# Optimization experiments

Hardware: AMD Instinct MI355X
Metric: run time of the kernel (lower is better)

The kernel has to match this reference:

```python
import jax, jax.numpy as jnp
import numpy as np

B, T, S = 2, 1024, 1024
D_Q, D_KV, D_OUT = 2048, 2048, 2048
N_Q, N_KV, H = 16, 4, 128
G = N_Q // N_KV  # GQA groups
MIN_TS, MAX_TS = 1.0, 10000.0
SDPA_SCALE = 1.0  # dia uses scale=1.0 in F.scaled_dot_product_attention


def setup_inputs() -> dict:
    key = jax.random.key(0)
    ks = jax.random.split(key, 6)
    Xq = jax.random.normal(ks[0], (B, T, D_Q), jnp.float32)
    Xkv = jax.random.normal(ks[1], (B, S, D_KV), jnp.float32)
    q_positions = jnp.broadcast_to(jnp.arange(T, dtype=jnp.int32), (B, T))
    kv_positions = jnp.broadcast_to(jnp.arange(S, dtype=jnp.int32), (B, S))
    Wq = jax.random.normal(ks[2], (D_Q, N_Q, H), jnp.float32) * (D_Q ** -0.5)
    Wk = jax.random.normal(ks[3], (D_KV, N_KV, H), jnp.float32) * (D_KV ** -0.5)
    Wv = jax.random.normal(ks[4], (D_KV, N_KV, H), jnp.float32) * (D_KV ** -0.5)
    Wo = jax.random.normal(ks[5], (N_Q, H, D_OUT), jnp.float32) * ((N_Q * H) ** -0.5)
    return {"Xq": Xq, "Xkv": Xkv, "q_positions": q_positions,
            "kv_positions": kv_positions, "Wq": Wq, "Wk": Wk, "Wv": Wv, "Wo": Wo}


def _apply_rope(x, positions):
    # x: (B, L, N, H); positions: (B, L) int
    half = H // 2
    fraction = 2.0 * jnp.arange(half, dtype=jnp.float32) / H
    timescale = MIN_TS * (MAX_TS / MIN_TS) ** fraction  # (half,)
    sinusoid = positions.astype(jnp.float32)[:, :, None, None] / timescale  # (B,L,1,half)
    sin, cos = jnp.sin(sinusoid), jnp.cos(sinusoid)
    x = x.astype(jnp.float32)
    x1, x2 = jnp.split(x, 2, axis=-1)
    return jnp.concatenate([x1 * cos - x2 * sin, x2 * cos + x1 * sin], axis=-1)


def reference(Xq, Xkv, q_positions, kv_positions, Wq, Wk, Wv, Wo):
    # QKV projections (DenseGeneral): (B,L,D) x (D,N,H) -> (B,L,N,H)
    q = jnp.einsum('btd,dnh->btnh', Xq, Wq)
    k = jnp.einsum('bsd,dnh->bsnh', Xkv, Wk)
    v = jnp.einsum('bsd,dnh->bsnh', Xkv, Wv)
    # RoPE on q and k
    q = _apply_rope(q, q_positions)
    k = _apply_rope(k, kv_positions)
    # GQA attention, scale = 1.0 (as in dia), no mask, non-causal
    q = q.transpose(0, 2, 1, 3).reshape(B, N_KV, G, T, H)  # (B,K,G,T,H)
    k = k.transpose(0, 2, 1, 3)                             # (B,K,S,H)
    v = v.transpose(0, 2, 1, 3)                             # (B,K,S,H)
    scores = jnp.einsum('bkgth,bksh->bkgts', q, k) * SDPA_SCALE
    probs = jax.nn.softmax(scores, axis=-1)
    attn = jnp.einsum('bkgts,bksh->bkgth', probs, v)        # (B,K,G,T,H)
    attn = attn.reshape(B, N_Q, T, H).transpose(0, 2, 1, 3)  # (B,T,N,H)
    # Output projection (DenseGeneral contracting (N,H))
    out = jnp.einsum('btnh,nho->bto', attn, Wo)
    return out
```

## Files before the change

kernel.cpp:

```cpp
#include <hip/hip_runtime.h>
#include <hip/hip_bf16.h>
#include <math.h>
#include <stdint.h>

#define B_SZ 2
#define T_SZ 1024
#define S_SZ 1024
#define NQ 16
#define NKV 4
#define HD 128
#define DQ 2048
#define DKV 2048
#define DOUT 2048

typedef _Float16 half8 __attribute__((ext_vector_type(8)));
typedef _Float16 half4 __attribute__((ext_vector_type(4)));
typedef float f32x4 __attribute__((ext_vector_type(4)));

__device__ __forceinline__ half8 load8_f16(const _Float16* p) {
    return *reinterpret_cast<const half8*>(p);
}

__device__ __forceinline__ void stage16(const _Float16* g, _Float16* l, int lane) {
#if __has_builtin(__builtin_amdgcn_global_load_lds)
    __builtin_amdgcn_global_load_lds(
        (const __attribute__((address_space(1))) uint32_t*)g,
        (__attribute__((address_space(3))) uint32_t*)l, 16, 0, 0);
#else
    *reinterpret_cast<half8*>(l + lane * 8) = *reinterpret_cast<const half8*>(g);
#endif
}

__device__ __forceinline__ void conv_blk(const float* __restrict__ in,
                                         _Float16* __restrict__ out, int vb) {
    size_t i = ((size_t)vb * 256 + threadIdx.x) * 8;
    float4 a = *reinterpret_cast<const float4*>(in + i);
    float4 b = *reinterpret_cast<const float4*>(in + i + 4);
    half8 r;
    r[0] = (_Float16)a.x; r[1] = (_Float16)a.y; r[2] = (_Float16)a.z; r[3] = (_Float16)a.w;
    r[4] = (_Float16)b.x; r[5] = (_Float16)b.y; r[6] = (_Float16)b.z; r[7] = (_Float16)b.w;
    *reinterpret_cast<half8*>(out + i) = r;
}

__device__ __forceinline__ void tr_blk(const float* __restrict__ in,
                                       _Float16* __restrict__ out,
                                       int R, int C, int bx, int by,
                                       _Float16 (*tile)[72]) {
    const int tx = threadIdx.x & 15, ty = threadIdx.x >> 4;
    const int r0 = by * 64, c0 = bx * 64;
    #pragma unroll
    for (int i = 0; i < 4; ++i) {
        int r = ty + i * 16;
        float4 v = *reinterpret_cast<const float4*>(&in[(size_t)(r0 + r) * C + c0 + tx * 4]);
        tile[r][tx * 4 + 0] = (_Float16)v.x;
        tile[r][tx * 4 + 1] = (_Float16)v.y;
        tile[r][tx * 4 + 2] = (_Float16)v.z;
        tile[r][tx * 4 + 3] = (_Float16)v.w;
    }
    __syncthreads();
    #pragma unroll
    for (int i = 0; i < 4; ++i) {
        int oc = ty + i * 16;
        half4 v;
        v[0] = tile[tx * 4 + 0][oc];
        v[1] = tile[tx * 4 + 1][oc];
        v[2] = tile[tx * 4 + 2][oc];
        v[3] = tile[tx * 4 + 3][oc];
        *reinterpret_cast<half4*>(&out[(size_t)(c0 + oc) * R + r0 + tx * 4]) = v;
    }
}

__device__ __forceinline__ void tr16_blk(const _Float16* __restrict__ in,
                                         _Float16* __restrict__ out,
                                         int Cin, int Cout, int r0, int c0,
                                         _Float16 (*tile)[72]) {
    const int tx = threadIdx.x & 15, ty = threadIdx.x >> 4;
    #pragma unroll
    for (int i = 0; i < 4; ++i) {
        int r = ty + i * 16;
        half4 v = *reinterpret_cast<const half4*>(&in[(size_t)(r0 + r) * Cin + c0 + tx * 4]);
        tile[r][tx * 4 + 0] = v[0];
        tile[r][tx * 4 + 1] = v[1];
        tile[r][tx * 4 + 2] = v[2];
        tile[r][tx * 4 + 3] = v[3];
    }
    __syncthreads();
    #pragma unroll
    for (int i = 0; i < 4; ++i) {
        int oc = ty + i * 16;
        half4 v;
        v[0] = tile[tx * 4 + 0][oc];
        v[1] = tile[tx * 4 + 1][oc];
        v[2] = tile[tx * 4 + 2][oc];
        v[3] = tile[tx * 4 + 3][oc];
        *reinterpret_cast<half4*>(&out[(size_t)(c0 + oc) * Cout + r0 + tx * 4]) = v;
    }
}

__device__ __forceinline__ void rope_blk(_Float16* __restrict__ x,
                                         const int* __restrict__ pos,
                                         int N, int rowStride, int vb) {
    size_t idx = (size_t)vb * 256 + threadIdx.x;
    int h = (int)(idx & 63);
    size_t g = idx >> 6;
    int n = (int)(g % (size_t)N);
    size_t bl = g / (size_t)N;
    float p = (float)pos[bl];
    float ts = powf(10000.f, (float)h * (1.f / 64.f));
    float ang = p / ts;
    float s = sinf(ang), c = cosf(ang);
    size_t base = bl * (size_t)rowStride + (size_t)n * HD;
    float x1 = (float)x[base + h];
    float x2 = (float)x[base + h + 64];
    x[base + h]      = (_Float16)(x1 * c - x2 * s);
    x[base + h + 64] = (_Float16)(x2 * c + x1 * s);
}

__global__ __launch_bounds__(256) void prep1(const float* __restrict__ Xq, _Float16* __restrict__ Xq16,
                                             const float* __restrict__ Xkv, _Float16* __restrict__ Xkv16,
                                             const float* __restrict__ Wq, _Float16* __restrict__ WqT,
                                             const float* __restrict__ Wk, const float* __restrict__ Wv,
                                             _Float16* __restrict__ WkvT) {
    __shared__ _Float16 tile[64][72];
    int bx = blockIdx.x;
    if (bx < 2048) { conv_blk(Xq, Xq16, bx); return; }
    bx -= 2048;
    if (bx < 2048) { conv_blk(Xkv, Xkv16, bx); return; }
    bx -= 2048;
    if (bx < 1024) { tr_blk(Wq, WqT, 2048, 2048, bx & 31, bx >> 5, tile); return; }
    bx -= 1024;
    if (bx < 256) { tr_blk(Wk, WkvT, 2048, 512, bx & 7, bx >> 3, tile); return; }
    bx -= 256;
    tr_blk(Wv, WkvT + (size_t)512 * 2048, 2048, 512, bx & 7, bx >> 3, tile);
}

__global__ __launch_bounds__(256) void prep2(const float* __restrict__ Wo, _Float16* __restrict__ WoT,
                                             _Float16* __restrict__ Qh, const int* __restrict__ qpos,
                                             _Float16* __restrict__ KVh, const int* __restrict__ kpos,
                                             _Float16* __restrict__ VTh) {
    __shared__ _Float16 tile[64][72];
    int bx = blockIdx.x;
    if (bx < 1024) { tr_blk(Wo, WoT, 2048, 2048, bx & 31, bx >> 5, tile); return; }
    bx -= 1024;
    if (bx < 8192) { rope_blk(Qh, qpos, NQ, NQ * HD, bx); return; }
    bx -= 8192;
    if (bx < 2048) { rope_blk(KVh, kpos, NKV, 1024, bx); return; }
    bx -= 2048;
    {
        const int head = bx >> 5;
        const int t = bx & 31;
        const int sx = t & 15, hx = t >> 4;
        const int b = head >> 2, kn = head & 3;
        const _Float16* in = KVh + (size_t)(b * S_SZ) * 1024 + 512 + kn * HD;
        _Float16* out = VTh + (size_t)head * HD * S_SZ;
        tr16_blk(in, out, 1024, 1024, sx * 64, hx * 64, tile);
    }
}

template <int BM, int BN, typename TC>
__device__ __forceinline__ void gemm_tile(const _Float16* __restrict__ A,
                                          const _Float16* __restrict__ Bt,
                                          TC* __restrict__ C,
                                          int N, int K, int kbeg, int kend,
                                          int bm, int bn, _Float16* lds) {
    constexpr int ASEG = BM / 8, BSEG = BN / 8, TSEG = ASEG + BSEG, PSEG = TSEG / 4;
    constexpr int BUFSZ = TSEG * 512;
    const int tid = threadIdx.x, lane = tid & 63, w = tid >> 6;
    const int quad = lane >> 4, l16 = lane & 15;
    constexpr int WM = BM / 2, WN = BN / 2, MI = WM / 16, NI = WN / 16;
    const int wm = (w >> 1) * WM, wn = (w & 1) * WN;

    const int srl = lane >> 3;
    const int skb = (lane & 7) ^ srl;

    const _Float16* gp[PSEG];
    _Float16* lp[PSEG];
    #pragma unroll
    for (int p = 0; p < PSEG; ++p) {
        int s = w + p * 4;
        if (s < ASEG) {
            gp[p] = A + (size_t)(bm + s * 8 + srl) * K + kbeg + skb * 8;
        } else {
            gp[p] = Bt + (size_t)(bn + (s - ASEG) * 8 + srl) * K + kbeg + skb * 8;
        }
        lp[p] = lds + s * 512;
    }

    f32x4 acc[MI][NI];
    #pragma unroll
    for (int i = 0; i < MI; ++i)
        #pragma unroll
        for (int j = 0; j < NI; ++j)
            acc[i][j] = (f32x4){0.f, 0.f, 0.f, 0.f};

    const int nsteps = (kend - kbeg) >> 6;

    #pragma unroll
    for (int p = 0; p < PSEG; ++p)
        stage16(gp[p], lp[p], lane);
    __syncthreads();

    const int rxa = l16 & 7;
    int cur = 0;
    for (int it = 0; it < nsteps; ++it) {
        if (it + 1 < nsteps) {
            const int ko = (it + 1) * 64;
            const int nb = (cur ^ 1) * BUFSZ;
            #pragma unroll
            for (int p = 0; p < PSEG; ++p)
                stage16(gp[p] + ko, lp[p] + nb, lane);
        }
        const _Float16* lb = lds + cur * BUFSZ;
        #pragma unroll
        for (int h = 0; h < 2; ++h) {
            const int kb0 = h * 4 + quad;
            const int kswz = (kb0 ^ rxa) * 8;
            half8 af[MI], bf[NI];
            #pragma unroll
            for (int i = 0; i < MI; ++i) {
                const int r = wm + 16 * i + l16;
                af[i] = *reinterpret_cast<const half8*>(&lb[r * 64 + kswz]);
            }
            #pragma unroll
            for (int j = 0; j < NI; ++j) {
                const int r = wn + 16 * j + l16;
                bf[j] = *reinterpret_cast<const half8*>(&lb[BM * 64 + r * 64 + kswz]);
            }
            #pragma unroll
            for (int i = 0; i < MI; ++i)
                #pragma unroll
                for (int j = 0; j < NI; ++j)
                    acc[i][j] = __builtin_amdgcn_mfma_f32_16x16x32_f16(af[i], bf[j], acc[i][j], 0, 0, 0);
        }
        __syncthreads();
        cur ^= 1;
    }

    #pragma unroll
    for (int i = 0; i < MI; ++i)
        #pragma unroll
        for (int j = 0; j < NI; ++j)
            #pragma unroll
            for (int r = 0; r < 4; ++r) {
                size_t idx = (size_t)(bm + wm + 16 * i + quad * 4 + r) * N + bn + wn + 16 * j + l16;
                C[idx] = (TC)acc[i][j][r];
            }
}

__global__ __launch_bounds__(256) void proj_fused(const _Float16* __restrict__ Xq,
                                                  const _Float16* __restrict__ WqT,
                                                  _Float16* __restrict__ Qh,
                                                  const _Float16* __restrict__ Xkv,
                                                  const _Float16* __restrict__ WkvT,
                                                  _Float16* __restrict__ KVh) {
    __shared__ __align__(16) _Float16 lds[2 * (128 + 64) * 64];
    int bx = blockIdx.x;
    if (bx < 512) {
        gemm_tile<128, 64, _Float16>(Xq, WqT, Qh, 2048, 2048, 0, 2048,
                                     (bx & 15) * 128, (bx >> 4) * 64, lds);
    } else {
        bx -= 512;
        gemm_tile<128, 64, _Float16>(Xkv, WkvT, KVh, 1024, 2048, 0, 2048,
                                     (bx & 15) * 128, (bx >> 4) * 64, lds);
    }
}

__global__ __launch_bounds__(256) void gemm_out(const _Float16* __restrict__ A,
                                                const _Float16* __restrict__ Bt,
                                                float* __restrict__ C) {
    __shared__ __align__(16) _Float16 lds[2 * (128 + 64) * 64];
    const int bx = blockIdx.x;
    gemm_tile<128, 64, float>(A, Bt, C, 2048, 2048, 0, 2048,
                              (bx & 15) * 128, (bx >> 4) * 64, lds);
}

__global__ __launch_bounds__(256) void attn_kernel(const _Float16* __restrict__ Q,
                                                   const _Float16* __restrict__ KV,
                                                   const _Float16* __restrict__ VT,
                                                   _Float16* __restrict__ O) {
    constexpr int KBUF = 64 * 128;
    constexpr int VBUF = 128 * 64;
    constexpr int BUFSZ = KBUF + VBUF;
    __shared__ __align__(16) _Float16 lds[2 * BUFSZ];
    __shared__ __align__(16) _Float16 Ps[4][16][72];
    const int tid = threadIdx.x, lane = tid & 63, w = tid >> 6;
    const int quad = lane >> 4, l16 = lane & 15;
    const int blk = blockIdx.x;
    const int t0 = (blk & 15) * 64;
    const int n  = (blk >> 4) & 15;
    const int b  = blk >> 8;
    const int kn = n >> 2;
    const _Float16* KVb  = KV + (size_t)b * S_SZ * 1024 + kn * HD;
    const _Float16* Vhead = VT + (size_t)(b * NKV + kn) * HD * S_SZ;

    const int krow_i = lane >> 4;
    const int kcp    = lane & 15;
    const int vrow_i = lane >> 3;
    const int vcp    = lane & 7;

    half8 qf[4];
    #pragma unroll
    for (int kh = 0; kh < 4; ++kh)
        qf[kh] = load8_f16(&Q[(((size_t)b * T_SZ + t0 + w * 16 + l16) * NQ + n) * HD + kh * 32 + quad * 8]);

    f32x4 o_acc[8];
    #pragma unroll
    for (int i = 0; i < 8; ++i) o_acc[i] = (f32x4){0.f, 0.f, 0.f, 0.f};
    float m_row[4] = {-1e30f, -1e30f, -1e30f, -1e30f};
    float l_part[4] = {0.f, 0.f, 0.f, 0.f};

    auto stage_tile = [&](int s0, int buf) {
        _Float16* kb = lds + buf * BUFSZ;
        _Float16* vb = kb + KBUF;
        #pragma unroll
        for (int j = 0; j < 4; ++j) {
            const int s = w + j * 4;
            const int row = 4 * s + krow_i;
            const int kc = kcp ^ (row & 7);
            stage16(KVb + (size_t)(s0 + row) * 1024 + kc * 8, kb + s * 512, lane);
        }
        #pragma unroll
        for (int j = 0; j < 4; ++j) {
            const int s = w + j * 4;
            const int row = 8 * s + vrow_i;
            const int vc = vcp ^ (row & 7);
            stage16(Vhead + (size_t)row * S_SZ + s0 + vc * 8, vb + s * 512, lane);
        }
    };

    stage_tile(0, 0);
    __syncthreads();

    const int rx = l16 & 7;
    int cur = 0;
    for (int t = 0; t < S_SZ / 64; ++t) {
        if (t + 1 < S_SZ / 64)
            stage_tile((t + 1) * 64, cur ^ 1);
        const _Float16* Kb = lds + cur * BUFSZ;
        const _Float16* Vb = Kb + KBUF;

        f32x4 sf[4];
        __builtin_amdgcn_s_setprio(1);
        #pragma unroll
        for (int i4 = 0; i4 < 4; ++i4) {
            const int srow = i4 * 16 + l16;
            f32x4 sa = (f32x4){0.f, 0.f, 0.f, 0.f};
            #pragma unroll
            for (int kh = 0; kh < 4; ++kh) {
                const int c = kh * 4 + quad;
                half8 bk = *reinterpret_cast<const half8*>(
                    &Kb[srow * 128 + ((c ^ rx) * 8)]);
                sa = __builtin_amdgcn_mfma_f32_16x16x32_f16(qf[kh], bk, sa, 0, 0, 0);
            }
            sf[i4] = sa;
        }
        __builtin_amdgcn_s_setprio(0);

        float mc[4];
        #pragma unroll
        for (int r = 0; r < 4; ++r) {
            float m0 = fmaxf(fmaxf(sf[0][r], sf[1][r]), fmaxf(sf[2][r], sf[3][r]));
            #pragma unroll
            for (int off = 1; off < 16; off <<= 1)
                m0 = fmaxf(m0, __shfl_xor(m0, off, 64));
            mc[r] = m0;
        }
        bool grow = (mc[0] > m_row[0]) | (mc[1] > m_row[1]) |
                    (mc[2] > m_row[2]) | (mc[3] > m_row[3]);
        if (__any(grow)) {
            #pragma unroll
            for (int r = 0; r < 4; ++r) {
                float mn = fmaxf(m_row[r], mc[r]);
                float alpha = __expf(m_row[r] - mn);
                m_row[r] = mn;
                l_part[r] *= alpha;
                #pragma unroll
                for (int ht = 0; ht < 8; ++ht)
                    o_acc[ht][r] *= alpha;
            }
        }
        #pragma unroll
        for (int r = 0; r < 4; ++r) {
            float p0 = __expf(sf[0][r] - m_row[r]);
            float p1 = __expf(sf[1][r] - m_row[r]);
            float p2 = __expf(sf[2][r] - m_row[r]);
            float p3 = __expf(sf[3][r] - m_row[r]);
            l_part[r] += (p0 + p1) + (p2 + p3);
            Ps[w][quad * 4 + r][l16]      = (_Float16)p0;
            Ps[w][quad * 4 + r][16 + l16] = (_Float16)p1;
            Ps[w][quad * 4 + r][32 + l16] = (_Float16)p2;
            Ps[w][quad * 4 + r][48 + l16] = (_Float16)p3;
        }
        __builtin_amdgcn_wave_barrier();
        half8 ap0 = *reinterpret_cast<const half8*>(&Ps[w][l16][quad * 8]);
        half8 ap1 = *reinterpret_cast<const half8*>(&Ps[w][l16][32 + quad * 8]);
        __builtin_amdgcn_wave_barrier();
        __builtin_amdgcn_s_setprio(1);
        #pragma unroll
        for (int ht = 0; ht < 8; ++ht) {
            const int vrow = ht * 16 + l16;
            half8 bv0 = *reinterpret_cast<const half8*>(
                &Vb[vrow * 64 + ((quad ^ rx) * 8)]);
            o_acc[ht] = __builtin_amdgcn_mfma_f32_16x16x32_f16(ap0, bv0, o_acc[ht], 0, 0, 0);
            half8 bv1 = *reinterpret_cast<const half8*>(
                &Vb[vrow * 64 + (((4 + quad) ^ rx) * 8)]);
            o_acc[ht] = __builtin_amdgcn_mfma_f32_16x16x32_f16(ap1, bv1, o_acc[ht], 0, 0, 0);
        }
        __builtin_amdgcn_s_setprio(0);

        __syncthreads();
        cur ^= 1;
    }

    float inv_l[4];
    #pragma unroll
    for (int r = 0; r < 4; ++r) {
        float l = l_part[r];
        #pragma unroll
        for (int off = 1; off < 16; off <<= 1)
            l += __shfl_xor(l, off, 64);
        inv_l[r] = 1.f / fmaxf(l, 1e-30f);
    }
    #pragma unroll
    for (int ht = 0; ht < 8; ++ht)
        #pragma unroll
        for (int r = 0; r < 4; ++r)
            O[(((size_t)b * T_SZ + t0 + w * 16 + quad * 4 + r) * NQ + n) * HD + ht * 16 + l16] =
                (_Float16)(o_acc[ht][r] * inv_l[r]);
}

extern "C" void kernel_launch(void* const* d_in, const int* in_sizes, int n_in,
                              void* d_out, int out_size, void* d_ws, size_t ws_size,
                              hipStream_t stream) {
    const float* Xq   = (const float*)d_in[0];
    const float* Xkv  = (const float*)d_in[1];
    const int*   qpos = (const int*)d_in[2];
    const int*   kpos = (const int*)d_in[3];
    const float* Wq   = (const float*)d_in[4];
    const float* Wk   = (const float*)d_in[5];
    const float* Wv   = (const float*)d_in[6];
    const float* Wo   = (const float*)d_in[7];
    float* out = (float*)d_out;

    const size_t SZ8 = 8388608;
    uint8_t* ws = (uint8_t*)d_ws;
    _Float16* Xq16  = (_Float16*)(ws);
    _Float16* Xkv16 = (_Float16*)(ws + SZ8);
    _Float16* WqT   = (_Float16*)(ws + 2 * SZ8);
    _Float16* WkvT  = (_Float16*)(ws + 3 * SZ8);
    _Float16* Qh    = (_Float16*)(ws + 3 * SZ8 + 4194304);
    _Float16* Ah  = Xq16;
    _Float16* WoT = Xkv16;
    _Float16* KVh = WqT;
    _Float16* VTh = WkvT;

    dim3 blk(256);
    prep1<<<5632, blk, 0, stream>>>(Xq, Xq16, Xkv, Xkv16, Wq, WqT, Wk, Wv, WkvT);
    proj_fused<<<768, blk, 0, stream>>>(Xq16, WqT, Qh, Xkv16, WkvT, KVh);
    prep2<<<11520, blk, 0, stream>>>(Wo, WoT, Qh, qpos, KVh, kpos, VTh);
    attn_kernel<<<512, blk, 0, stream>>>(Qh, KVh, VTh, Ah);
    gemm_out<<<512, blk, 0, stream>>>(Ah, WoT, out);
}
```

Before: 233.0 us.

## Vectorize RoPE with shared trig, remap attention blocks, lazy softmax rescale

RoPE now has each thread compute sin/cos for four frequencies once, using exp2 and fast intrinsics, and apply them across several heads with half4 vector loads and stores. This cuts the prep2 grid from 11520 blocks to 2048. The attention kernel remaps block indices so neighbouring blocks land on different XCDs or share KV heads. The online softmax skips rescaling unless the running max grows by more than 8, which avoids exp and multiply work but risks fp16 P-value overflow and uses approximate trig.

```diff
diff --git a/kernel.cpp b/kernel.cpp
--- a/kernel.cpp
+++ b/kernel.cpp
@@ -97,23 +97,38 @@
     }
 }
 
-__device__ __forceinline__ void rope_blk(_Float16* __restrict__ x,
-                                         const int* __restrict__ pos,
-                                         int N, int rowStride, int vb) {
-    size_t idx = (size_t)vb * 256 + threadIdx.x;
-    int h = (int)(idx & 63);
-    size_t g = idx >> 6;
-    int n = (int)(g % (size_t)N);
-    size_t bl = g / (size_t)N;
-    float p = (float)pos[bl];
-    float ts = powf(10000.f, (float)h * (1.f / 64.f));
-    float ang = p / ts;
-    float s = sinf(ang), c = cosf(ang);
-    size_t base = bl * (size_t)rowStride + (size_t)n * HD;
-    float x1 = (float)x[base + h];
-    float x2 = (float)x[base + h + 64];
-    x[base + h]      = (_Float16)(x1 * c - x2 * s);
-    x[base + h + 64] = (_Float16)(x2 * c + x1 * s);
+template <int NHEADS, int NSLOT, int RS>
+__device__ __forceinline__ void rope_fast(_Float16* __restrict__ x,
+                                          const int* __restrict__ pos, int vb) {
+    const int t = vb * 256 + (int)threadIdx.x;
+    const int hq = t & 15;
+    const int ns = (t >> 4) % NSLOT;
+    const int bl = (t >> 4) / NSLOT;
+    const float p = (float)pos[bl];
+    const float C = -0.2076205059304601f;
+    float s[4], c[4];
+    #pragma unroll
+    for (int j = 0; j < 4; ++j) {
+        float ang = p * exp2f((float)(hq * 4 + j) * C);
+        s[j] = __sinf(ang);
+        c[j] = __cosf(ang);
+    }
+    #pragma unroll
+    for (int i = 0; i < NHEADS / NSLOT; ++i) {
+        const int n = ns + i * NSLOT;
+        size_t base = (size_t)bl * RS + (size_t)n * HD + hq * 4;
+        half4 a  = *reinterpret_cast<half4*>(&x[base]);
+        half4 b2 = *reinterpret_cast<half4*>(&x[base + 64]);
+        half4 o1, o2;
+        #pragma unroll
+        for (int j = 0; j < 4; ++j) {
+            float x1 = (float)a[j], x2 = (float)b2[j];
+            o1[j] = (_Float16)(x1 * c[j] - x2 * s[j]);
+            o2[j] = (_Float16)(x2 * c[j] + x1 * s[j]);
+        }
+        *reinterpret_cast<half4*>(&x[base])      = o1;
+        *reinterpret_cast<half4*>(&x[base + 64]) = o2;
+    }
 }
 
 __global__ __launch_bounds__(256) void prep1(const float* __restrict__ Xq, _Float16* __restrict__ Xq16,
@@ -142,10 +157,10 @@
     int bx = blockIdx.x;
     if (bx < 1024) { tr_blk(Wo, WoT, 2048, 2048, bx & 31, bx >> 5, tile); return; }
     bx -= 1024;
-    if (bx < 8192) { rope_blk(Qh, qpos, NQ, NQ * HD, bx); return; }
-    bx -= 8192;
-    if (bx < 2048) { rope_blk(KVh, kpos, NKV, 1024, bx); return; }
-    bx -= 2048;
+    if (bx < 512) { rope_fast<NQ, 4, NQ * HD>(Qh, qpos, bx); return; }
+    bx -= 512;
+    if (bx < 256) { rope_fast<NKV, 2, 1024>(KVh, kpos, bx); return; }
+    bx -= 256;
     {
         const int head = bx >> 5;
         const int t = bx & 31;
@@ -285,7 +300,8 @@
     __shared__ __align__(16) _Float16 Ps[4][16][72];
     const int tid = threadIdx.x, lane = tid & 63, w = tid >> 6;
     const int quad = lane >> 4, l16 = lane & 15;
-    const int blk = blockIdx.x;
+    const int hw = blockIdx.x;
+    const int blk = (hw & 7) * 64 + (hw >> 3);
     const int t0 = (blk & 15) * 64;
     const int n  = (blk >> 4) & 15;
     const int b  = blk >> 8;
@@ -365,8 +381,8 @@
                 m0 = fmaxf(m0, __shfl_xor(m0, off, 64));
             mc[r] = m0;
         }
-        bool grow = (mc[0] > m_row[0]) | (mc[1] > m_row[1]) |
-                    (mc[2] > m_row[2]) | (mc[3] > m_row[3]);
+        bool grow = (mc[0] > m_row[0] + 8.f) | (mc[1] > m_row[1] + 8.f) |
+                    (mc[2] > m_row[2] + 8.f) | (mc[3] > m_row[3] + 8.f);
         if (__any(grow)) {
             #pragma unroll
             for (int r = 0; r < 4; ++r) {
@@ -457,7 +473,7 @@
     dim3 blk(256);
     prep1<<<5632, blk, 0, stream>>>(Xq, Xq16, Xkv, Xkv16, Wq, WqT, Wk, Wv, WkvT);
     proj_fused<<<768, blk, 0, stream>>>(Xq16, WqT, Qh, Xkv16, WkvT, KVh);
-    prep2<<<11520, blk, 0, stream>>>(Wo, WoT, Qh, qpos, KVh, kpos, VTh);
+    prep2<<<2048, blk, 0, stream>>>(Wo, WoT, Qh, qpos, KVh, kpos, VTh);
     attn_kernel<<<512, blk, 0, stream>>>(Qh, KVh, VTh, Ah);
     gemm_out<<<512, blk, 0, stream>>>(Ah, WoT, out);
 }
```

New measurement: 219.1 us. -6.0%, faster.
